# Kernel optimization log

Measured on AMD Instinct MI355X. Metric: run time of the kernel, lower is better.

The kernel has to match this reference:

```python
import jax, jax.numpy as jnp
import numpy as np

D = 32          # embedding_size
B = 16384       # batch_size
P = 16          # neighbor_sample_size (paths per item per hop)
NE = 100000     # n_entity
NU = 100000     # n_user
NR = 32         # n_relation
N_ITER = 2


def setup_inputs() -> dict:
    key = jax.random.key(0)
    ks = jax.random.split(key, 20)
    s = 0.1
    nrm = lambda k, sh: jax.random.normal(k, sh, dtype=jnp.float32) * s
    inp = {
        "user_table": nrm(ks[0], (NU, D)),
        "ent_table": nrm(ks[1], (NE, D)),
        "rel_table": nrm(ks[2], (NR, D)),
        # PyTorch LSTM params, gate order (i, f, g, o)
        "w_ih0": nrm(ks[3], (4 * D, 2 * D)),
        "w_hh0": nrm(ks[4], (4 * D, D)),
        "b_ih0": nrm(ks[5], (4 * D,)),
        "b_hh0": nrm(ks[6], (4 * D,)),
        "w_ih1": nrm(ks[7], (4 * D, 2 * D)),
        "w_hh1": nrm(ks[8], (4 * D, D)),
        "b_ih1": nrm(ks[9], (4 * D,)),
        "b_hh1": nrm(ks[10], (4 * D,)),
        "agg_w": nrm(ks[11], (D, D)),
        "agg_b": nrm(ks[12], (D,)),
        "users": jax.random.randint(ks[13], (B,), 0, NU),
        "items": jax.random.randint(ks[14], (B,), 0, NE),
        "ratings": jax.random.randint(ks[15], (B,), 0, 2),
        # hop h path table: [n_entity, P, 2*(h+1)+1]; values < 32 valid for both tables
        "lp0": jax.random.randint(ks[16], (NE, P, 3), 0, 32),
        "lp1": jax.random.randint(ks[17], (NE, P, 5), 0, 32),
    }
    return inp


def _lstm_last(seq, w_ih, w_hh, b_ih, b_hh):
    # seq: [N, T, 2D] -> final hidden state [N, D], PyTorch gate order i,f,g,o
    N = seq.shape[0]
    H = w_hh.shape[1]
    bias = b_ih + b_hh

    def step(carry, x):
        h, c = carry
        g = x @ w_ih.T + h @ w_hh.T + bias
        i, f, gg, o = jnp.split(g, 4, axis=-1)
        c = jax.nn.sigmoid(f) * c + jax.nn.sigmoid(i) * jnp.tanh(gg)
        h = jax.nn.sigmoid(o) * jnp.tanh(c)
        return (h, c), None

    h0 = jnp.zeros((N, H), seq.dtype)
    (h, _), _ = jax.lax.scan(step, (h0, h0), jnp.swapaxes(seq, 0, 1))
    return h


def _forward(user_table, ent_table, rel_table, lstm_params, agg_w, agg_b,
             users, items, ratings, lps):
    u = user_table[users]                # [B, D]
    items_emb = ent_table[items]         # [B, D]
    for hop in range(N_ITER):
        lp = lps[hop]
        w_ih, w_hh, b_ih, b_hh = lstm_params[hop]
        il = lp[items]                   # [B, P, 2*(hop+1)+1]
        seed_e = ent_table[il[:, :, 0]]  # [B, P, D]
        u_b = jnp.broadcast_to(u[:, None, :], seed_e.shape)
        first = jnp.concatenate([u_b, seed_e], -1)[:, :, None, :]   # [B,P,1,2D]
        rel_e = rel_table[il[:, :, 1::2]]                            # [B,P,hop+1,D]
        tail_e = ent_table[il[:, :, 2::2]]                           # [B,P,hop+1,D]
        rest = jnp.concatenate([rel_e, tail_e], -1)                  # [B,P,hop+1,2D]
        seq = jnp.concatenate([first, rest], 2).reshape(B * P, hop + 2, 2 * D)
        h = _lstm_last(seq, w_ih, w_hh, b_ih, b_hh)                  # [B*P, D]
        final = h.reshape(B, P, D).sum(axis=1)                       # hidden_out sum
        items_emb = (items_emb + final) @ agg_w.T + agg_b            # 'sum' aggregator
    scores = jnp.sum(u * items_emb, axis=-1)                         # [B]
    r = ratings.astype(scores.dtype)
    # stable BCE on sigmoid(scores)
    loss = -jnp.mean(r * jax.nn.log_sigmoid(scores) + (1.0 - r) * jax.nn.log_sigmoid(-scores))
    return loss, jax.nn.sigmoid(scores)


def reference(user_table, ent_table, rel_table,
              w_ih0, w_hh0, b_ih0, b_hh0,
              w_ih1, w_hh1, b_ih1, b_hh1,
              agg_w, agg_b,
              users, items, ratings, lp0, lp1):
    lstm_params = [(w_ih0, w_hh0, b_ih0, b_hh0), (w_ih1, w_hh1, b_ih1, b_hh1)]
    loss, scores_normalized = _forward(user_table, ent_table, rel_table,
                                       lstm_params, agg_w, agg_b,
                                       users, items, ratings, (lp0, lp1))
    return (loss, scores_normalized, items)
```

## Files before the change

kernel.cpp:

```cpp
#include <hip/hip_runtime.h>
#include <math.h>

#define D  32
#define BN 16384
#define PP 16

typedef __bf16 bf16x8 __attribute__((ext_vector_type(8)));
typedef float  floatx4 __attribute__((ext_vector_type(4)));

#define WIH_OFF     0
#define WHH_OFF     18432
#define BIAS_OFF    28672
#define IMG_BYTES   29184
#define H_OFF       IMG_BYTES
#define LDS_BYTES   (IMG_BYTES + 5120)

#define K1 1.44269504088896341f
#define K2 2.88539008177792681f

__device__ __forceinline__ float sigf(float x) {
    float e = __builtin_amdgcn_exp2f(-x * K1);
    return __builtin_amdgcn_rcpf(1.0f + e);
}
__device__ __forceinline__ float logsigf(float x) {
    float ax = fabsf(x);
    float l = log1pf(__expf(-ax));
    return (x >= 0.0f) ? -l : x - l;
}

__device__ __forceinline__ bf16x8 cvt8(float4 lo, float4 hi) {
    bf16x8 r = { (__bf16)lo.x, (__bf16)lo.y, (__bf16)lo.z, (__bf16)lo.w,
                 (__bf16)hi.x, (__bf16)hi.y, (__bf16)hi.z, (__bf16)hi.w };
    return r;
}
__device__ __forceinline__ bf16x8 load_frag(const float* __restrict__ tab,
                                            int row, int ak) {
    const float4* p = (const float4*)(tab + (size_t)row * D) + (ak >> 2);
    return cvt8(p[0], p[1]);
}

__global__ __launch_bounds__(256)
void prep_weights(const float* __restrict__ w_ih0, const float* __restrict__ w_hh0,
                  const float* __restrict__ b_ih0, const float* __restrict__ b_hh0,
                  const float* __restrict__ w_ih1, const float* __restrict__ w_hh1,
                  const float* __restrict__ b_ih1, const float* __restrict__ b_hh1,
                  float* __restrict__ img0, float* __restrict__ img1)
{
    const bool second = blockIdx.x >= 8;
    const float* w_ih = second ? w_ih1 : w_ih0;
    const float* w_hh = second ? w_hh1 : w_hh0;
    const float* b_ih = second ? b_ih1 : b_ih0;
    const float* b_hh = second ? b_hh1 : b_hh0;
    char* base = (char*)(second ? img1 : img0);
    const int t0 = (blockIdx.x & 7) * 256 + threadIdx.x;
    for (int idx = t0; idx < 8192; idx += 2048) {
        int n = idx >> 6, k = idx & 63;
        ((__bf16*)(base + WIH_OFF))[n * 72 + k] = (__bf16)w_ih[idx];
    }
    for (int idx = t0; idx < 4096; idx += 2048) {
        int n = idx >> 5, k = idx & 31;
        ((__bf16*)(base + WHH_OFF))[n * 40 + k] = (__bf16)w_hh[idx];
    }
    if (t0 < 128)
        ((float*)(base + BIAS_OFF))[t0] = b_ih[t0] + b_hh[t0];
}

template<bool FIRST, bool LAST>
__device__ __forceinline__ void lstm_step(
    const char* __restrict__ Wih, const char* __restrict__ Whh, char* __restrict__ Hl,
    bf16x8 ax0, bf16x8 ax1, const float* __restrict__ biasv,
    float* __restrict__ cst, float* __restrict__ hout,
    int bnl, int ak, int am, int wrow, int lane)
{
    bf16x8 ah = {};
    if (!FIRST) ah = *(const bf16x8*)(Hl + am * 80 + ak * 2);

    floatx4 acc[8];
    #pragma unroll
    for (int nt = 0; nt < 8; ++nt) {
        floatx4 v = { biasv[nt], biasv[nt], biasv[nt], biasv[nt] };
        acc[nt] = v;
    }
    #pragma unroll
    for (int nt = 0; nt < 8; ++nt) {
        const int bn = nt * 16 + bnl;
        bf16x8 b0 = *(const bf16x8*)(Wih + bn * 144 + ak * 2);
        bf16x8 b1 = *(const bf16x8*)(Wih + bn * 144 + 64 + ak * 2);
        floatx4 a = acc[nt];
        a = __builtin_amdgcn_mfma_f32_16x16x32_bf16(ax0, b0, a, 0, 0, 0);
        a = __builtin_amdgcn_mfma_f32_16x16x32_bf16(ax1, b1, a, 0, 0, 0);
        if (!FIRST) {
            bf16x8 bh = *(const bf16x8*)(Whh + bn * 80 + ak * 2);
            a = __builtin_amdgcn_mfma_f32_16x16x32_bf16(ah, bh, a, 0, 0, 0);
        }
        acc[nt] = a;
    }

    #pragma unroll
    for (int ng = 0; ng < 2; ++ng) {
        floatx4 gi = acc[ng], gf = acc[ng + 2], gg = acc[ng + 4], go = acc[ng + 6];
        #pragma unroll
        for (int r = 0; r < 4; ++r) {
            float Ai = 1.0f + __builtin_amdgcn_exp2f(-gi[r] * K1);
            float Af = 1.0f + __builtin_amdgcn_exp2f(-gf[r] * K1);
            float G2 = __builtin_amdgcn_exp2f(gg[r] * K2);
            float Gp = G2 + 1.0f, Gm = G2 - 1.0f;
            float cold = FIRST ? 0.0f : cst[ng * 4 + r];
            float num = cold * Ai * Gp + Gm * Af;
            float c = num * __builtin_amdgcn_rcpf(Af * Ai * Gp);
            cst[ng * 4 + r] = c;
            float Ao = 1.0f + __builtin_amdgcn_exp2f(-go[r] * K1);
            float C2 = __builtin_amdgcn_exp2f(c * K2);
            float h = (C2 - 1.0f) * __builtin_amdgcn_rcpf(Ao * (C2 + 1.0f));
            hout[ng * 4 + r] = h;
            if (!LAST) {
                int pr = wrow + (lane >> 4) * 4 + r;
                *(__bf16*)(Hl + pr * 80 + (ng * 16 + bnl) * 2) = (__bf16)h;
            }
        }
    }
}

__global__ __launch_bounds__(256, 2)
void hop_mfma(const float* __restrict__ user_table,
              const float* __restrict__ ent_table,
              const float* __restrict__ rel_table,
              const float* __restrict__ img0,
              const float* __restrict__ img1,
              const int*   __restrict__ users,
              const int*   __restrict__ items,
              const int*   __restrict__ lp0,
              const int*   __restrict__ lp1,
              float* __restrict__ F0,
              float* __restrict__ F1)
{
    __shared__ __align__(16) char lds[LDS_BYTES];

    const bool second = blockIdx.x & 1;
    const int  idx    = blockIdx.x >> 1;
    const int tid  = threadIdx.x;
    const int lane = tid & 63;
    const int wave = tid >> 6;

    {
        const float4* g = (const float4*)(second ? img1 : img0);
        float4* l = (float4*)lds;
        #pragma unroll
        for (int i = 0; i < 8; ++i) {
            int k = i * 256 + tid;
            if (k < IMG_BYTES / 16) l[k] = g[k];
        }
    }

    const char* Wih = lds + WIH_OFF;
    const char* Whh = lds + WHH_OFF;
    char* Hl = lds + H_OFF;

    const int bnl  = lane & 15;
    const int ak   = (lane >> 4) * 8;
    const int wrow = wave * 16;
    const int am   = wrow + bnl;

    const int fb   = idx * 4 + wave;
    const int item = items[fb];
    const int user = users[fb];
    const int* __restrict__ il = (second ? lp1 : lp0)
        + ((size_t)item * PP + bnl) * (second ? 5 : 3);

    bf16x8 xa0, xb0, xa1, xb1, xa2 = {}, xb2 = {};
    {
        const int i0 = il[0];
        xa0 = load_frag(user_table, user, ak);
        xb0 = load_frag(ent_table, i0, ak);
        const int i1 = il[1], i2 = il[2];
        xa1 = load_frag(rel_table, i1, ak);
        xb1 = load_frag(ent_table, i2, ak);
        if (second) {
            const int i3 = il[3], i4 = il[4];
            xa2 = load_frag(rel_table, i3, ak);
            xb2 = load_frag(ent_table, i4, ak);
        }
    }

    __syncthreads();

    float biasv[8];
    {
        const float* bias = (const float*)(lds + BIAS_OFF);
        #pragma unroll
        for (int nt = 0; nt < 8; ++nt) biasv[nt] = bias[nt * 16 + bnl];
    }

    float cst[8], hout[8];
    lstm_step<true, false>(Wih, Whh, Hl, xa0, xb0, biasv, cst, hout, bnl, ak, am, wrow, lane);
    if (!second) {
        lstm_step<false, true>(Wih, Whh, Hl, xa1, xb1, biasv, cst, hout, bnl, ak, am, wrow, lane);
    } else {
        lstm_step<false, false>(Wih, Whh, Hl, xa1, xb1, biasv, cst, hout, bnl, ak, am, wrow, lane);
        lstm_step<false, true >(Wih, Whh, Hl, xa2, xb2, biasv, cst, hout, bnl, ak, am, wrow, lane);
    }

    float* Fout = second ? F1 : F0;
    #pragma unroll
    for (int ng = 0; ng < 2; ++ng) {
        float v = hout[ng * 4 + 0] + hout[ng * 4 + 1] + hout[ng * 4 + 2] + hout[ng * 4 + 3];
        v += __shfl_xor(v, 16);
        v += __shfl_xor(v, 32);
        if (lane < 16)
            Fout[(size_t)fb * D + ng * 16 + lane] = v;
    }
}

__global__ __launch_bounds__(256)
void chain_score(const float* __restrict__ user_table,
                 const float* __restrict__ ent_table,
                 const float* __restrict__ agg_w,
                 const float* __restrict__ agg_b,
                 const int*   __restrict__ users,
                 const int*   __restrict__ items,
                 const int*   __restrict__ ratings,
                 const float* __restrict__ F0,
                 const float* __restrict__ F1,
                 float* __restrict__ out,
                 float* __restrict__ partials)
{
    __shared__ float s[8][33];
    __shared__ float red[8];
    const int tid = threadIdx.x;
    const int bb  = tid >> 5;
    const int j   = tid & 31;
    const int b   = blockIdx.x * 8 + bb;
    const int it  = items[b];

    s[bb][j] = ent_table[(size_t)it * D + j] + F0[(size_t)b * D + j];
    __syncthreads();
    const float* __restrict__ w = agg_w + (size_t)j * D;
    float e0 = agg_b[j];
    #pragma unroll
    for (int k = 0; k < D; ++k) e0 = fmaf(s[bb][k], w[k], e0);
    __syncthreads();
    s[bb][j] = e0 + F1[(size_t)b * D + j];
    __syncthreads();
    float e1 = agg_b[j];
    #pragma unroll
    for (int k = 0; k < D; ++k) e1 = fmaf(s[bb][k], w[k], e1);

    float prod = user_table[(size_t)users[b] * D + j] * e1;
    #pragma unroll
    for (int m = 1; m < 32; m <<= 1) prod += __shfl_xor(prod, m);
    if (j == 0) {
        out[1 + b]      = sigf(prod);
        out[1 + BN + b] = (float)it;
        float r = (float)ratings[b];
        red[bb] = r * logsigf(prod) + (1.0f - r) * logsigf(-prod);
    }
    __syncthreads();
    if (tid == 0) {
        float t = 0.0f;
        #pragma unroll
        for (int q = 0; q < 8; ++q) t += red[q];
        partials[blockIdx.x] = t;
    }
}

__global__ __launch_bounds__(256)
void loss_kernel(const float* __restrict__ partials, float* __restrict__ out)
{
    __shared__ float red[4];
    const int t = threadIdx.x;
    float v = 0.0f;
    #pragma unroll
    for (int q = 0; q < 8; ++q) v += partials[q * 256 + t];
    #pragma unroll
    for (int m = 1; m < 64; m <<= 1) v += __shfl_xor(v, m);
    if ((t & 63) == 0) red[t >> 6] = v;
    __syncthreads();
    if (t == 0) out[0] = -(red[0] + red[1] + red[2] + red[3]) / (float)BN;
}

extern "C" void kernel_launch(void* const* d_in, const int* in_sizes, int n_in,
                              void* d_out, int out_size, void* d_ws, size_t ws_size,
                              hipStream_t stream)
{
    const float* user_table = (const float*)d_in[0];
    const float* ent_table  = (const float*)d_in[1];
    const float* rel_table  = (const float*)d_in[2];
    const float* w_ih0 = (const float*)d_in[3];
    const float* w_hh0 = (const float*)d_in[4];
    const float* b_ih0 = (const float*)d_in[5];
    const float* b_hh0 = (const float*)d_in[6];
    const float* w_ih1 = (const float*)d_in[7];
    const float* w_hh1 = (const float*)d_in[8];
    const float* b_ih1 = (const float*)d_in[9];
    const float* b_hh1 = (const float*)d_in[10];
    const float* agg_w = (const float*)d_in[11];
    const float* agg_b = (const float*)d_in[12];
    const int* users   = (const int*)d_in[13];
    const int* items   = (const int*)d_in[14];
    const int* ratings = (const int*)d_in[15];
    const int* lp0     = (const int*)d_in[16];
    const int* lp1     = (const int*)d_in[17];
    float* out = (float*)d_out;

    float* ws       = (float*)d_ws;
    float* F0       = ws;
    float* F1       = ws + (size_t)BN * D;
    float* partials = ws + 2 * (size_t)BN * D;
    float* img0     = ws + 2 * (size_t)BN * D + 2048;
    float* img1     = img0 + IMG_BYTES / 4;

    prep_weights<<<16, 256, 0, stream>>>(w_ih0, w_hh0, b_ih0, b_hh0,
                                         w_ih1, w_hh1, b_ih1, b_hh1, img0, img1);
    hop_mfma<<<8192, 256, 0, stream>>>(
        user_table, ent_table, rel_table, img0, img1,
        users, items, lp0, lp1, F0, F1);
    chain_score<<<BN / 8, 256, 0, stream>>>(
        user_table, ent_table, agg_w, agg_b, users, items, ratings,
        F0, F1, out, partials);
    loss_kernel<<<1, 256, 0, stream>>>(partials, out);
}
```

Baseline: 254.3 us.

## Process two batch elements per wave to amortize weight staging and interleave MFMAs

Each wave now handles two independent batch rows (A and B), so every block covers 8 rows instead of 4 and the grid is halved. Weight fragments loaded from LDS are reused for both rows, and the two independent MFMA chains are interleaved to hide MFMA latency. The per-block cost of copying the ~29KB weight image into LDS is paid half as often. In exchange, register pressure roughly doubles and LDS grows by another hidden-state buffer, which may lower occupancy under the 2-blocks-per-SM launch bound.

```diff
diff --git a/kernel.cpp b/kernel.cpp
--- a/kernel.cpp
+++ b/kernel.cpp
@@ -12,8 +12,9 @@
 #define WHH_OFF     18432
 #define BIAS_OFF    28672
 #define IMG_BYTES   29184
-#define H_OFF       IMG_BYTES
-#define LDS_BYTES   (IMG_BYTES + 5120)
+#define HA_OFF      IMG_BYTES
+#define HB_OFF      (IMG_BYTES + 5120)
+#define LDS_BYTES   (IMG_BYTES + 10240)
 
 #define K1 1.44269504088896341f
 #define K2 2.88539008177792681f
@@ -66,56 +67,75 @@
 }
 
 template<bool FIRST, bool LAST>
-__device__ __forceinline__ void lstm_step(
-    const char* __restrict__ Wih, const char* __restrict__ Whh, char* __restrict__ Hl,
-    bf16x8 ax0, bf16x8 ax1, const float* __restrict__ biasv,
-    float* __restrict__ cst, float* __restrict__ hout,
+__device__ __forceinline__ void lstm_step2(
+    const char* __restrict__ Wih, const char* __restrict__ Whh,
+    char* __restrict__ HlA, char* __restrict__ HlB,
+    bf16x8 axA0, bf16x8 axA1, bf16x8 axB0, bf16x8 axB1,
+    const float* __restrict__ biasv,
+    float* __restrict__ cstA, float* __restrict__ cstB,
+    float* __restrict__ houtA, float* __restrict__ houtB,
     int bnl, int ak, int am, int wrow, int lane)
 {
-    bf16x8 ah = {};
-    if (!FIRST) ah = *(const bf16x8*)(Hl + am * 80 + ak * 2);
-
-    floatx4 acc[8];
+    bf16x8 ahA = {}, ahB = {};
+    if (!FIRST) {
+        ahA = *(const bf16x8*)(HlA + am * 80 + ak * 2);
+        ahB = *(const bf16x8*)(HlB + am * 80 + ak * 2);
+    }
+
+    floatx4 accA[8], accB[8];
     #pragma unroll
     for (int nt = 0; nt < 8; ++nt) {
         floatx4 v = { biasv[nt], biasv[nt], biasv[nt], biasv[nt] };
-        acc[nt] = v;
+        accA[nt] = v;
+        accB[nt] = v;
     }
     #pragma unroll
     for (int nt = 0; nt < 8; ++nt) {
         const int bn = nt * 16 + bnl;
         bf16x8 b0 = *(const bf16x8*)(Wih + bn * 144 + ak * 2);
         bf16x8 b1 = *(const bf16x8*)(Wih + bn * 144 + 64 + ak * 2);
-        floatx4 a = acc[nt];
-        a = __builtin_amdgcn_mfma_f32_16x16x32_bf16(ax0, b0, a, 0, 0, 0);
-        a = __builtin_amdgcn_mfma_f32_16x16x32_bf16(ax1, b1, a, 0, 0, 0);
+        floatx4 a = accA[nt], b = accB[nt];
+        a = __builtin_amdgcn_mfma_f32_16x16x32_bf16(axA0, b0, a, 0, 0, 0);
+        b = __builtin_amdgcn_mfma_f32_16x16x32_bf16(axB0, b0, b, 0, 0, 0);
+        a = __builtin_amdgcn_mfma_f32_16x16x32_bf16(axA1, b1, a, 0, 0, 0);
+        b = __builtin_amdgcn_mfma_f32_16x16x32_bf16(axB1, b1, b, 0, 0, 0);
         if (!FIRST) {
             bf16x8 bh = *(const bf16x8*)(Whh + bn * 80 + ak * 2);
-            a = __builtin_amdgcn_mfma_f32_16x16x32_bf16(ah, bh, a, 0, 0, 0);
-        }
-        acc[nt] = a;
+            a = __builtin_amdgcn_mfma_f32_16x16x32_bf16(ahA, bh, a, 0, 0, 0);
+            b = __builtin_amdgcn_mfma_f32_16x16x32_bf16(ahB, bh, b, 0, 0, 0);
+        }
+        accA[nt] = a;
+        accB[nt] = b;
     }
 
     #pragma unroll
     for (int ng = 0; ng < 2; ++ng) {
-        floatx4 gi = acc[ng], gf = acc[ng + 2], gg = acc[ng + 4], go = acc[ng + 6];
         #pragma unroll
         for (int r = 0; r < 4; ++r) {
-            float Ai = 1.0f + __builtin_amdgcn_exp2f(-gi[r] * K1);
-            float Af = 1.0f + __builtin_amdgcn_exp2f(-gf[r] * K1);
-            float G2 = __builtin_amdgcn_exp2f(gg[r] * K2);
-            float Gp = G2 + 1.0f, Gm = G2 - 1.0f;
-            float cold = FIRST ? 0.0f : cst[ng * 4 + r];
-            float num = cold * Ai * Gp + Gm * Af;
-            float c = num * __builtin_amdgcn_rcpf(Af * Ai * Gp);
-            cst[ng * 4 + r] = c;
-            float Ao = 1.0f + __builtin_amdgcn_exp2f(-go[r] * K1);
-            float C2 = __builtin_amdgcn_exp2f(c * K2);
-            float h = (C2 - 1.0f) * __builtin_amdgcn_rcpf(Ao * (C2 + 1.0f));
-            hout[ng * 4 + r] = h;
-            if (!LAST) {
-                int pr = wrow + (lane >> 4) * 4 + r;
-                *(__bf16*)(Hl + pr * 80 + (ng * 16 + bnl) * 2) = (__bf16)h;
+            #pragma unroll
+            for (int cc = 0; cc < 2; ++cc) {
+                floatx4* acc = cc ? accB : accA;
+                float* cst   = cc ? cstB : cstA;
+                float* hout  = cc ? houtB : houtA;
+                char*  Hl    = cc ? HlB : HlA;
+                float gi = acc[ng][r], gf = acc[ng + 2][r],
+                      gg = acc[ng + 4][r], go = acc[ng + 6][r];
+                float Ai = 1.0f + __builtin_amdgcn_exp2f(-gi * K1);
+                float Af = 1.0f + __builtin_amdgcn_exp2f(-gf * K1);
+                float G2 = __builtin_amdgcn_exp2f(gg * K2);
+                float Gp = G2 + 1.0f, Gm = G2 - 1.0f;
+                float cold = FIRST ? 0.0f : cst[ng * 4 + r];
+                float num = cold * Ai * Gp + Gm * Af;
+                float c = num * __builtin_amdgcn_rcpf(Af * Ai * Gp);
+                cst[ng * 4 + r] = c;
+                float Ao = 1.0f + __builtin_amdgcn_exp2f(-go * K1);
+                float C2 = __builtin_amdgcn_exp2f(c * K2);
+                float h = (C2 - 1.0f) * __builtin_amdgcn_rcpf(Ao * (C2 + 1.0f));
+                hout[ng * 4 + r] = h;
+                if (!LAST) {
+                    int pr = wrow + (lane >> 4) * 4 + r;
+                    *(__bf16*)(Hl + pr * 80 + (ng * 16 + bnl) * 2) = (__bf16)h;
+                }
             }
         }
     }
@@ -154,31 +174,38 @@
 
     const char* Wih = lds + WIH_OFF;
     const char* Whh = lds + WHH_OFF;
-    char* Hl = lds + H_OFF;
+    char* HlA = lds + HA_OFF;
+    char* HlB = lds + HB_OFF;
 
     const int bnl  = lane & 15;
     const int ak   = (lane >> 4) * 8;
     const int wrow = wave * 16;
     const int am   = wrow + bnl;
 
-    const int fb   = idx * 4 + wave;
-    const int item = items[fb];
-    const int user = users[fb];
-    const int* __restrict__ il = (second ? lp1 : lp0)
-        + ((size_t)item * PP + bnl) * (second ? 5 : 3);
-
-    bf16x8 xa0, xb0, xa1, xb1, xa2 = {}, xb2 = {};
+    const int fbA = idx * 8 + wave;
+    const int fbB = idx * 8 + 4 + wave;
+    const int L   = second ? 5 : 3;
+    const int* __restrict__ ilA = (second ? lp1 : lp0)
+        + ((size_t)items[fbA] * PP + bnl) * L;
+    const int* __restrict__ ilB = (second ? lp1 : lp0)
+        + ((size_t)items[fbB] * PP + bnl) * L;
+
+    bf16x8 xaA0, xbA0, xaA1, xbA1, xaA2 = {}, xbA2 = {};
+    bf16x8 xaB0, xbB0, xaB1, xbB1, xaB2 = {}, xbB2 = {};
     {
-        const int i0 = il[0];
-        xa0 = load_frag(user_table, user, ak);
-        xb0 = load_frag(ent_table, i0, ak);
-        const int i1 = il[1], i2 = il[2];
-        xa1 = load_frag(rel_table, i1, ak);
-        xb1 = load_frag(ent_table, i2, ak);
+        xaA0 = load_frag(user_table, users[fbA], ak);
+        xaB0 = load_frag(user_table, users[fbB], ak);
+        xbA0 = load_frag(ent_table, ilA[0], ak);
+        xbB0 = load_frag(ent_table, ilB[0], ak);
+        xaA1 = load_frag(rel_table, ilA[1], ak);
+        xaB1 = load_frag(rel_table, ilB[1], ak);
+        xbA1 = load_frag(ent_table, ilA[2], ak);
+        xbB1 = load_frag(ent_table, ilB[2], ak);
         if (second) {
-            const int i3 = il[3], i4 = il[4];
-            xa2 = load_frag(rel_table, i3, ak);
-            xb2 = load_frag(ent_table, i4, ak);
+            xaA2 = load_frag(rel_table, ilA[3], ak);
+            xaB2 = load_frag(rel_table, ilB[3], ak);
+            xbA2 = load_frag(ent_table, ilA[4], ak);
+            xbB2 = load_frag(ent_table, ilB[4], ak);
         }
     }
 
@@ -191,23 +218,32 @@
         for (int nt = 0; nt < 8; ++nt) biasv[nt] = bias[nt * 16 + bnl];
     }
 
-    float cst[8], hout[8];
-    lstm_step<true, false>(Wih, Whh, Hl, xa0, xb0, biasv, cst, hout, bnl, ak, am, wrow, lane);
+    float cstA[8], cstB[8], houtA[8], houtB[8];
+    lstm_step2<true, false>(Wih, Whh, HlA, HlB, xaA0, xbA0, xaB0, xbB0,
+                            biasv, cstA, cstB, houtA, houtB, bnl, ak, am, wrow, lane);
     if (!second) {
-        lstm_step<false, true>(Wih, Whh, Hl, xa1, xb1, biasv, cst, hout, bnl, ak, am, wrow, lane);
+        lstm_step2<false, true>(Wih, Whh, HlA, HlB, xaA1, xbA1, xaB1, xbB1,
+                                biasv, cstA, cstB, houtA, houtB, bnl, ak, am, wrow, lane);
     } else {
-        lstm_step<false, false>(Wih, Whh, Hl, xa1, xb1, biasv, cst, hout, bnl, ak, am, wrow, lane);
-        lstm_step<false, true >(Wih, Whh, Hl, xa2, xb2, biasv, cst, hout, bnl, ak, am, wrow, lane);
+        lstm_step2<false, false>(Wih, Whh, HlA, HlB, xaA1, xbA1, xaB1, xbB1,
+                                 biasv, cstA, cstB, houtA, houtB, bnl, ak, am, wrow, lane);
+        lstm_step2<false, true >(Wih, Whh, HlA, HlB, xaA2, xbA2, xaB2, xbB2,
+                                 biasv, cstA, cstB, houtA, houtB, bnl, ak, am, wrow, lane);
     }
 
     float* Fout = second ? F1 : F0;
     #pragma unroll
     for (int ng = 0; ng < 2; ++ng) {
-        float v = hout[ng * 4 + 0] + hout[ng * 4 + 1] + hout[ng * 4 + 2] + hout[ng * 4 + 3];
-        v += __shfl_xor(v, 16);
-        v += __shfl_xor(v, 32);
-        if (lane < 16)
-            Fout[(size_t)fb * D + ng * 16 + lane] = v;
+        float vA = houtA[ng * 4 + 0] + houtA[ng * 4 + 1] + houtA[ng * 4 + 2] + houtA[ng * 4 + 3];
+        float vB = houtB[ng * 4 + 0] + houtB[ng * 4 + 1] + houtB[ng * 4 + 2] + houtB[ng * 4 + 3];
+        vA += __shfl_xor(vA, 16);
+        vA += __shfl_xor(vA, 32);
+        vB += __shfl_xor(vB, 16);
+        vB += __shfl_xor(vB, 32);
+        if (lane < 16) {
+            Fout[(size_t)fbA * D + ng * 16 + lane] = vA;
+            Fout[(size_t)fbB * D + ng * 16 + lane] = vB;
+        }
     }
 }
 
@@ -311,7 +347,7 @@
 
     prep_weights<<<16, 256, 0, stream>>>(w_ih0, w_hh0, b_ih0, b_hh0,
                                          w_ih1, w_hh1, b_ih1, b_hh1, img0, img1);
-    hop_mfma<<<8192, 256, 0, stream>>>(
+    hop_mfma<<<4096, 256, 0, stream>>>(
         user_table, ent_table, rel_table, img0, img1,
         users, items, lp0, lp1, F0, F1);
     chain_score<<<BN / 8, 256, 0, stream>>>(
```

New measurement: 244.3 us. 3.9% less time.

## Transpose LSTM MFMA so weights stay in registers and paths map to N

Applied to the files above, without the earlier changes.

Swaps the MFMA operand roles so the gate weights become the A operand and are preloaded once per thread into registers (24 bf16x8 plus bias vectors), while path inputs become the B operand. This removes the per-step LDS weight reads. The weight LDS image is then reused as per-wave hidden-state scratch, and the output reduction changes to shuffles across the 16 path lanes with float4 stores. The cost is higher register pressure from the 24 resident weight fragments, which may limit occupancy at two blocks of 256 threads, and a different per-step layout for writing the hidden state.

```diff
diff --git a/kernel.cpp b/kernel.cpp
--- a/kernel.cpp
+++ b/kernel.cpp
@@ -6,14 +6,13 @@
 #define PP 16
 
 typedef __bf16 bf16x8 __attribute__((ext_vector_type(8)));
+typedef __bf16 bf16x4 __attribute__((ext_vector_type(4)));
 typedef float  floatx4 __attribute__((ext_vector_type(4)));
 
 #define WIH_OFF     0
 #define WHH_OFF     18432
 #define BIAS_OFF    28672
 #define IMG_BYTES   29184
-#define H_OFF       IMG_BYTES
-#define LDS_BYTES   (IMG_BYTES + 5120)
 
 #define K1 1.44269504088896341f
 #define K2 2.88539008177792681f
@@ -28,15 +27,13 @@
     return (x >= 0.0f) ? -l : x - l;
 }
 
-__device__ __forceinline__ bf16x8 cvt8(float4 lo, float4 hi) {
-    bf16x8 r = { (__bf16)lo.x, (__bf16)lo.y, (__bf16)lo.z, (__bf16)lo.w,
-                 (__bf16)hi.x, (__bf16)hi.y, (__bf16)hi.z, (__bf16)hi.w };
+__device__ __forceinline__ bf16x8 load_frag(const float* __restrict__ tab,
+                                            int row, int q) {
+    const float4* p = (const float4*)(tab + (size_t)row * D + q * 8);
+    float4 a = p[0], b = p[1];
+    bf16x8 r = { (__bf16)a.x, (__bf16)a.y, (__bf16)a.z, (__bf16)a.w,
+                 (__bf16)b.x, (__bf16)b.y, (__bf16)b.z, (__bf16)b.w };
     return r;
-}
-__device__ __forceinline__ bf16x8 load_frag(const float* __restrict__ tab,
-                                            int row, int ak) {
-    const float4* p = (const float4*)(tab + (size_t)row * D) + (ak >> 2);
-    return cvt8(p[0], p[1]);
 }
 
 __global__ __launch_bounds__(256)
@@ -67,57 +64,53 @@
 
 template<bool FIRST, bool LAST>
 __device__ __forceinline__ void lstm_step(
-    const char* __restrict__ Wih, const char* __restrict__ Whh, char* __restrict__ Hl,
-    bf16x8 ax0, bf16x8 ax1, const float* __restrict__ biasv,
-    float* __restrict__ cst, float* __restrict__ hout,
-    int bnl, int ak, int am, int wrow, int lane)
-{
-    bf16x8 ah = {};
-    if (!FIRST) ah = *(const bf16x8*)(Hl + am * 80 + ak * 2);
+    const bf16x8* __restrict__ Wa0, const bf16x8* __restrict__ Wa1,
+    const bf16x8* __restrict__ Wh,  const floatx4* __restrict__ biasv,
+    char* __restrict__ Hw, bf16x8 bx0, bf16x8 bx1,
+    float* __restrict__ cst, float* __restrict__ hlo, float* __restrict__ hhi,
+    int q, int bnl)
+{
+    bf16x8 bh = {};
+    if (!FIRST) bh = *(const bf16x8*)(Hw + bnl * 80 + q * 16);
 
     floatx4 acc[8];
     #pragma unroll
-    for (int nt = 0; nt < 8; ++nt) {
-        floatx4 v = { biasv[nt], biasv[nt], biasv[nt], biasv[nt] };
-        acc[nt] = v;
-    }
-    #pragma unroll
-    for (int nt = 0; nt < 8; ++nt) {
-        const int bn = nt * 16 + bnl;
-        bf16x8 b0 = *(const bf16x8*)(Wih + bn * 144 + ak * 2);
-        bf16x8 b1 = *(const bf16x8*)(Wih + bn * 144 + 64 + ak * 2);
-        floatx4 a = acc[nt];
-        a = __builtin_amdgcn_mfma_f32_16x16x32_bf16(ax0, b0, a, 0, 0, 0);
-        a = __builtin_amdgcn_mfma_f32_16x16x32_bf16(ax1, b1, a, 0, 0, 0);
-        if (!FIRST) {
-            bf16x8 bh = *(const bf16x8*)(Whh + bn * 80 + ak * 2);
-            a = __builtin_amdgcn_mfma_f32_16x16x32_bf16(ah, bh, a, 0, 0, 0);
-        }
-        acc[nt] = a;
-    }
-
-    #pragma unroll
-    for (int ng = 0; ng < 2; ++ng) {
-        floatx4 gi = acc[ng], gf = acc[ng + 2], gg = acc[ng + 4], go = acc[ng + 6];
+    for (int mt = 0; mt < 8; ++mt) acc[mt] = biasv[mt];
+    #pragma unroll
+    for (int mt = 0; mt < 8; ++mt) {
+        floatx4 a = acc[mt];
+        a = __builtin_amdgcn_mfma_f32_16x16x32_bf16(Wa0[mt], bx0, a, 0, 0, 0);
+        a = __builtin_amdgcn_mfma_f32_16x16x32_bf16(Wa1[mt], bx1, a, 0, 0, 0);
+        if (!FIRST)
+            a = __builtin_amdgcn_mfma_f32_16x16x32_bf16(Wh[mt], bh, a, 0, 0, 0);
+        acc[mt] = a;
+    }
+
+    #pragma unroll
+    for (int hf = 0; hf < 2; ++hf) {
+        float* hout = hf ? hhi : hlo;
         #pragma unroll
         for (int r = 0; r < 4; ++r) {
-            float Ai = 1.0f + __builtin_amdgcn_exp2f(-gi[r] * K1);
-            float Af = 1.0f + __builtin_amdgcn_exp2f(-gf[r] * K1);
-            float G2 = __builtin_amdgcn_exp2f(gg[r] * K2);
+            float gi = acc[0 + hf][r], gf = acc[2 + hf][r],
+                  gg = acc[4 + hf][r], go = acc[6 + hf][r];
+            float Ai = 1.0f + __builtin_amdgcn_exp2f(-gi * K1);
+            float Af = 1.0f + __builtin_amdgcn_exp2f(-gf * K1);
+            float G2 = __builtin_amdgcn_exp2f(gg * K2);
             float Gp = G2 + 1.0f, Gm = G2 - 1.0f;
-            float cold = FIRST ? 0.0f : cst[ng * 4 + r];
+            float cold = FIRST ? 0.0f : cst[hf * 4 + r];
             float num = cold * Ai * Gp + Gm * Af;
             float c = num * __builtin_amdgcn_rcpf(Af * Ai * Gp);
-            cst[ng * 4 + r] = c;
-            float Ao = 1.0f + __builtin_amdgcn_exp2f(-go[r] * K1);
+            cst[hf * 4 + r] = c;
+            float Ao = 1.0f + __builtin_amdgcn_exp2f(-go * K1);
             float C2 = __builtin_amdgcn_exp2f(c * K2);
-            float h = (C2 - 1.0f) * __builtin_amdgcn_rcpf(Ao * (C2 + 1.0f));
-            hout[ng * 4 + r] = h;
-            if (!LAST) {
-                int pr = wrow + (lane >> 4) * 4 + r;
-                *(__bf16*)(Hl + pr * 80 + (ng * 16 + bnl) * 2) = (__bf16)h;
-            }
+            hout[r] = (C2 - 1.0f) * __builtin_amdgcn_rcpf(Ao * (C2 + 1.0f));
         }
+    }
+    if (!LAST) {
+        bf16x4 plo = { (__bf16)hlo[0], (__bf16)hlo[1], (__bf16)hlo[2], (__bf16)hlo[3] };
+        bf16x4 phi = { (__bf16)hhi[0], (__bf16)hhi[1], (__bf16)hhi[2], (__bf16)hhi[3] };
+        *(bf16x4*)(Hw + bnl * 80 + 8 * q)      = plo;
+        *(bf16x4*)(Hw + bnl * 80 + 32 + 8 * q) = phi;
     }
 }
 
@@ -134,7 +127,7 @@
               float* __restrict__ F0,
               float* __restrict__ F1)
 {
-    __shared__ __align__(16) char lds[LDS_BYTES];
+    __shared__ __align__(16) char lds[IMG_BYTES];
 
     const bool second = blockIdx.x & 1;
     const int  idx    = blockIdx.x >> 1;
@@ -151,63 +144,65 @@
             if (k < IMG_BYTES / 16) l[k] = g[k];
         }
     }
-
-    const char* Wih = lds + WIH_OFF;
-    const char* Whh = lds + WHH_OFF;
-    char* Hl = lds + H_OFF;
-
-    const int bnl  = lane & 15;
-    const int ak   = (lane >> 4) * 8;
-    const int wrow = wave * 16;
-    const int am   = wrow + bnl;
+    __syncthreads();
+
+    const int bnl = lane & 15;
+    const int q   = lane >> 4;
+
+    bf16x8 Wa0[8], Wa1[8], Wh[8];
+    floatx4 biasv[8];
+    #pragma unroll
+    for (int mt = 0; mt < 8; ++mt) {
+        const int gr = 16 * mt + bnl;
+        Wa0[mt] = *(const bf16x8*)(lds + WIH_OFF + gr * 144 + q * 16);
+        Wa1[mt] = *(const bf16x8*)(lds + WIH_OFF + gr * 144 + 64 + q * 16);
+        Wh[mt]  = *(const bf16x8*)(lds + WHH_OFF + gr * 80 + q * 16);
+        biasv[mt] = *(const floatx4*)(lds + BIAS_OFF + (16 * mt + 4 * q) * 4);
+    }
+    __syncthreads();
+
+    char* Hw = lds + wave * 1280;
 
     const int fb   = idx * 4 + wave;
     const int item = items[fb];
     const int user = users[fb];
+    const int L    = second ? 5 : 3;
     const int* __restrict__ il = (second ? lp1 : lp0)
-        + ((size_t)item * PP + bnl) * (second ? 5 : 3);
-
-    bf16x8 xa0, xb0, xa1, xb1, xa2 = {}, xb2 = {};
-    {
-        const int i0 = il[0];
-        xa0 = load_frag(user_table, user, ak);
-        xb0 = load_frag(ent_table, i0, ak);
-        const int i1 = il[1], i2 = il[2];
-        xa1 = load_frag(rel_table, i1, ak);
-        xb1 = load_frag(ent_table, i2, ak);
-        if (second) {
-            const int i3 = il[3], i4 = il[4];
-            xa2 = load_frag(rel_table, i3, ak);
-            xb2 = load_frag(ent_table, i4, ak);
+        + ((size_t)item * PP + bnl) * L;
+
+    bf16x8 bx0s0, bx1s0, bx0s1, bx1s1, bx0s2 = {}, bx1s2 = {};
+    bx0s0 = load_frag(user_table, user, q);
+    bx1s0 = load_frag(ent_table, il[0], q);
+    bx0s1 = load_frag(rel_table, il[1], q);
+    bx1s1 = load_frag(ent_table, il[2], q);
+    if (second) {
+        bx0s2 = load_frag(rel_table, il[3], q);
+        bx1s2 = load_frag(ent_table, il[4], q);
+    }
+
+    float cst[8], hlo[4], hhi[4];
+    lstm_step<true, false>(Wa0, Wa1, Wh, biasv, Hw, bx0s0, bx1s0, cst, hlo, hhi, q, bnl);
+    if (!second) {
+        lstm_step<false, true>(Wa0, Wa1, Wh, biasv, Hw, bx0s1, bx1s1, cst, hlo, hhi, q, bnl);
+    } else {
+        lstm_step<false, false>(Wa0, Wa1, Wh, biasv, Hw, bx0s1, bx1s1, cst, hlo, hhi, q, bnl);
+        lstm_step<false, true >(Wa0, Wa1, Wh, biasv, Hw, bx0s2, bx1s2, cst, hlo, hhi, q, bnl);
+    }
+
+    #pragma unroll
+    for (int r = 0; r < 4; ++r) {
+        #pragma unroll
+        for (int m = 1; m < 16; m <<= 1) {
+            hlo[r] += __shfl_xor(hlo[r], m);
+            hhi[r] += __shfl_xor(hhi[r], m);
         }
     }
-
-    __syncthreads();
-
-    float biasv[8];
-    {
-        const float* bias = (const float*)(lds + BIAS_OFF);
-        #pragma unroll
-        for (int nt = 0; nt < 8; ++nt) biasv[nt] = bias[nt * 16 + bnl];
-    }
-
-    float cst[8], hout[8];
-    lstm_step<true, false>(Wih, Whh, Hl, xa0, xb0, biasv, cst, hout, bnl, ak, am, wrow, lane);
-    if (!second) {
-        lstm_step<false, true>(Wih, Whh, Hl, xa1, xb1, biasv, cst, hout, bnl, ak, am, wrow, lane);
-    } else {
-        lstm_step<false, false>(Wih, Whh, Hl, xa1, xb1, biasv, cst, hout, bnl, ak, am, wrow, lane);
-        lstm_step<false, true >(Wih, Whh, Hl, xa2, xb2, biasv, cst, hout, bnl, ak, am, wrow, lane);
-    }
-
-    float* Fout = second ? F1 : F0;
-    #pragma unroll
-    for (int ng = 0; ng < 2; ++ng) {
-        float v = hout[ng * 4 + 0] + hout[ng * 4 + 1] + hout[ng * 4 + 2] + hout[ng * 4 + 3];
-        v += __shfl_xor(v, 16);
-        v += __shfl_xor(v, 32);
-        if (lane < 16)
-            Fout[(size_t)fb * D + ng * 16 + lane] = v;
+    if (bnl == 0) {
+        float* Fout = (second ? F1 : F0) + (size_t)fb * D;
+        float4 vlo = { hlo[0], hlo[1], hlo[2], hlo[3] };
+        float4 vhi = { hhi[0], hhi[1], hhi[2], hhi[3] };
+        *(float4*)(Fout + 4 * q)      = vlo;
+        *(float4*)(Fout + 16 + 4 * q) = vhi;
     }
 }
 
@@ -258,7 +253,7 @@
     if (tid == 0) {
         float t = 0.0f;
         #pragma unroll
-        for (int q = 0; q < 8; ++q) t += red[q];
+        for (int qq = 0; qq < 8; ++qq) t += red[qq];
         partials[blockIdx.x] = t;
     }
 }
@@ -270,7 +265,7 @@
     const int t = threadIdx.x;
     float v = 0.0f;
     #pragma unroll
-    for (int q = 0; q < 8; ++q) v += partials[q * 256 + t];
+    for (int qq = 0; qq < 8; ++qq) v += partials[qq * 256 + t];
     #pragma unroll
     for (int m = 1; m < 64; m <<= 1) v += __shfl_xor(v, m);
     if ((t & 63) == 0) red[t >> 6] = v;
```

New measurement: 262.9 us. 1.03x slower.
